# Kernel tuning notes

Measured on AMD Instinct MI355X. Metric: run time of the kernel, lower is better.

The kernel has to match this reference:

```python
import jax, jax.numpy as jnp
import numpy as np

H = 512
NHALF = 32  # N // 2 complex conjugate pairs
LLEN = 8192


def setup_inputs() -> dict:
    key = jax.random.key(0)
    k1, k2, k3 = jax.random.split(key, 3)
    # log_dt ~ uniform in [log(dt_min), log(dt_max)]
    log_dt = jax.random.uniform(k1, (H,), dtype=jnp.float32) * (
        np.log(0.1) - np.log(0.001)) + np.log(0.001)
    # C: complex randn stored as (H, NHALF, 2) real view
    C = jax.random.normal(k2, (H, NHALF, 2), dtype=jnp.float32)
    log_A_real = jnp.log(0.5 * jnp.ones((H, NHALF), dtype=jnp.float32))
    A_imag = np.pi * jnp.broadcast_to(
        jnp.arange(NHALF, dtype=jnp.float32), (H, NHALF))
    return {"C": C, "log_dt": log_dt, "log_A_real": log_A_real,
            "A_imag": A_imag, "L": LLEN}


def reference(C, log_dt, log_A_real, A_imag, L):
    # zoh discretization of diagonal SSM -> kernel K of shape (H, L)
    dt = jnp.exp(log_dt)                                  # (H,)
    Cc = (C[..., 0] + 1j * C[..., 1]).astype(jnp.complex64)  # (H, n)
    A = (-jnp.exp(log_A_real) + 1j * A_imag).astype(jnp.complex64)  # (H, n)
    dtA = A * dt[:, None]                                 # (H, n)
    t = jnp.arange(L, dtype=jnp.float32)                  # (L,)
    C_scaled = Cc * (jnp.exp(dtA) - 1.0) / A              # (H, n)
    # Vandermonde: exp(dtA)^t over length L, reduce over n
    T = jnp.exp(dtA[:, :, None] * t[None, None, :])       # (H, n, L) complex
    K = 2.0 * jnp.einsum('hn,hnl->hl', C_scaled, T).real  # (H, L)
    return K
```

## Files before the change

### kernel.cpp

```cpp
#include <hip/hip_runtime.h>
#include <math.h>

#define HDIM   512
#define NH     32
#define NP     16
#define LLEN   8192
#define BLOCK  256
#define LSPLIT 2
#define LPB    (LLEN / LSPLIT)
#define LPT    16

typedef float vf2 __attribute__((ext_vector_type(2)));

static __device__ inline vf2 pk_mul(vf2 a, vf2 b) {
    vf2 d; asm("v_pk_mul_f32 %0, %1, %2" : "=v"(d) : "v"(a), "v"(b)); return d;
}
static __device__ inline vf2 pk_add(vf2 a, vf2 b) {
    vf2 d; asm("v_pk_add_f32 %0, %1, %2" : "=v"(d) : "v"(a), "v"(b)); return d;
}
static __device__ inline vf2 pk_fma(vf2 a, vf2 b, vf2 c) {
    vf2 d; asm("v_pk_fma_f32 %0, %1, %2, %3" : "=v"(d) : "v"(a), "v"(b), "v"(c)); return d;
}
static __device__ inline vf2 pk_fms(vf2 a, vf2 b, vf2 c) {
    vf2 d; asm("v_pk_fma_f32 %0, %1, %2, %3 neg_lo:[0,0,1] neg_hi:[0,0,1]"
               : "=v"(d) : "v"(a), "v"(b), "v"(c)); return d;
}

__global__ __launch_bounds__(BLOCK) void s4d_kernel(
    const float* __restrict__ C,
    const float* __restrict__ log_dt,
    const float* __restrict__ log_A_real,
    const float* __restrict__ A_imag,
    float* __restrict__ out)
{
    __shared__ float4 tabA[NP + 1][16];
    __shared__ float4 tabB[NP + 1][16];
    __shared__ float4 s_w [NP + 1];
    __shared__ float4 s_pq[NP + 1];
    __shared__ float4 s_p2[NP + 1];

    const int h   = blockIdx.y;
    const int ls  = blockIdx.x;
    const int tid = threadIdx.x;

    {
        const int n = tid & 31;
        const int g = tid >> 5;
        const int P = n >> 1, o = n & 1;
        const double dt  = exp((double)log_dt[h]);
        const double Are = -exp((double)log_A_real[h * NH + n]);
        const double Aim = (double)A_imag[h * NH + n];
        const double dre = Are * dt, dim = Aim * dt;

        double s1, c1; sincos(dim, &s1, &c1);
        const double em  = exp(dre);
        const double w1r = em * c1, w1i = em * s1;

        float* tabAf = (float*)&tabA[0][0];
        float* tabBf = (float*)&tabB[0][0];

        if (g < 4) {
            const double nre = w1r - 1.0, nim = w1i;
            const double den = Are * Are + Aim * Aim;
            const double fre = (nre * Are + nim * Aim) / den;
            const double fim = (nim * Are - nre * Aim) / den;
            const double Cre = (double)C[(h * NH + n) * 2 + 0];
            const double Cim = (double)C[(h * NH + n) * 2 + 1];
            const double csr = 2.0 * (Cre * fre - Cim * fim);
            const double csi = 2.0 * (Cre * fim + Cim * fre);

            const int    i0   = g * 4;
            const double base = 16.0 * (double)i0;
            double s0, c0; sincos(dim * base, &s0, &c0);
            const double m0 = exp(dre * base);
            const double er = m0 * c0, ei = m0 * s0;
            double gr = csr * er - csi * ei;
            double gi = csr * ei + csi * er;
            double ss, cs; sincos(dim * 16.0, &ss, &cs);
            const double ms  = exp(dre * 16.0);
            const double str = ms * cs, sti = ms * ss;
            for (int k = 0; k < 4; ++k) {
                const int idx = (P * 16 + i0 + k) * 4;
                tabAf[idx + o]     = (float)gr;
                tabAf[idx + 2 + o] = (float)gi;
                const double t = gr * str - gi * sti;
                gi = gr * sti + gi * str;
                gr = t;
            }
        } else {
            const int    i0   = (g - 4) * 4;
            const double base = (double)(LPB * ls) + 256.0 * (double)i0;
            double s0, c0; sincos(dim * base, &s0, &c0);
            const double m0 = exp(dre * base);
            double er = m0 * c0, ei = m0 * s0;
            double ss, cs; sincos(dim * 256.0, &ss, &cs);
            const double ms  = exp(dre * 256.0);
            const double str = ms * cs, sti = ms * ss;
            for (int k = 0; k < 4; ++k) {
                const int idx = (P * 16 + i0 + k) * 4;
                tabBf[idx + o]     = (float)er;
                tabBf[idx + 2 + o] = (float)ei;
                const double t = er * str - ei * sti;
                ei = er * sti + ei * str;
                er = t;
            }
        }

        if (g == 0) {
            float* wf  = (float*)&s_w[0];
            float* pqf = (float*)&s_pq[0];
            float* p2f = (float*)&s_p2[0];
            const double p  = 2.0 * w1r;
            const double q  = em * em;
            const double p2 = 2.0 * (w1r * w1r - w1i * w1i);
            const double q2 = q * q;
            wf [P * 4 + o]     = (float)w1r;
            wf [P * 4 + 2 + o] = (float)w1i;
            pqf[P * 4 + o]     = (float)p;
            pqf[P * 4 + 2 + o] = (float)q;
            p2f[P * 4 + o]     = (float)p2;
            p2f[P * 4 + 2 + o] = (float)q2;
        }
    }
    __syncthreads();

    const int lo = tid & 15, hi = tid >> 4;

    vf2 acc[LPT];
#pragma unroll
    for (int l = 0; l < LPT; ++l) acc[l] = (vf2)(0.f);

    float4 a4 = tabA[0][lo], b4 = tabB[0][hi];
    float4 c0 = s_w[0], c1 = s_pq[0], c2 = s_p2[0];

#pragma unroll 2
    for (int P = 0; P < NP; ++P) {
        const float4 na = tabA[P + 1][lo], nb = tabB[P + 1][hi];
        const float4 n0 = s_w[P + 1], n1 = s_pq[P + 1], n2 = s_p2[P + 1];

        const vf2 Ax = {a4.x, a4.y}, Ay = {a4.z, a4.w};
        const vf2 Bx = {b4.x, b4.y}, By = {b4.z, b4.w};
        const vf2 wr = {c0.x, c0.y}, wi = {c0.z, c0.w};
        const vf2 p  = {c1.x, c1.y}, q  = {c1.z, c1.w};
        const vf2 p2 = {c2.x, c2.y}, q2 = {c2.z, c2.w};

        const vf2 Tr = pk_fms(Ax, Bx, pk_mul(Ay, By));
        const vf2 Ti = pk_fma(Ax, By, pk_mul(Ay, Bx));
        const vf2 y0 = Tr;
        const vf2 y1 = pk_fms(Tr, wr, pk_mul(Ti, wi));
        const vf2 y2 = pk_fms(p, y1, pk_mul(q, y0));
        const vf2 y3 = pk_fms(p, y2, pk_mul(q, y1));
        acc[0] = pk_add(acc[0], y0);
        acc[1] = pk_add(acc[1], y1);
        acc[2] = pk_add(acc[2], y2);
        acc[3] = pk_add(acc[3], y3);

        vf2 e0 = y0, e1 = y2, o0 = y1, o1 = y3;
#pragma unroll
        for (int m = 0; m < 6; ++m) {
            const vf2 e2 = pk_fms(p2, e1, pk_mul(q2, e0));
            const vf2 o2 = pk_fms(p2, o1, pk_mul(q2, o0));
            acc[4 + 2 * m] = pk_add(acc[4 + 2 * m], e2);
            acc[5 + 2 * m] = pk_add(acc[5 + 2 * m], o2);
            e0 = e1; e1 = e2;
            o0 = o1; o1 = o2;
        }
        a4 = na; b4 = nb; c0 = n0; c1 = n1; c2 = n2;
    }

    float* orow = out + (size_t)h * LLEN + ls * LPB + LPT * tid;
#pragma unroll
    for (int j = 0; j < 4; ++j) {
        *(float4*)(orow + 4 * j) = make_float4(
            acc[4*j+0].x + acc[4*j+0].y,
            acc[4*j+1].x + acc[4*j+1].y,
            acc[4*j+2].x + acc[4*j+2].y,
            acc[4*j+3].x + acc[4*j+3].y);
    }
}

extern "C" void kernel_launch(void* const* d_in, const int* in_sizes, int n_in,
                              void* d_out, int out_size, void* d_ws, size_t ws_size,
                              hipStream_t stream) {
    const float* C          = (const float*)d_in[0];
    const float* log_dt     = (const float*)d_in[1];
    const float* log_A_real = (const float*)d_in[2];
    const float* A_imag     = (const float*)d_in[3];
    float* out = (float*)d_out;

    dim3 grid(LSPLIT, HDIM);
    s4d_kernel<<<grid, BLOCK, 0, stream>>>(C, log_dt, log_A_real, A_imag, out);
}
```

Baseline: 76.77 us.

## Split double-precision table setup into separate precompute kernel feeding main kernel

Moves the per-head double-precision twiddle/table generation (sincos/exp) out of the main kernel into a separate kernel that writes the tables to workspace. It computes them once per head instead of once per L-split block, and uses repeated squaring instead of transcendental calls. The main kernel now only loads the tables from global memory into shared memory, and its launch bounds request higher occupancy. The cost is an extra kernel launch and a global-memory round trip. Long sequential complex-multiply chains in double precision replace the parallel sincos, which may also change accuracy slightly.

```diff
diff --git a/kernel.cpp b/kernel.cpp
--- a/kernel.cpp
+++ b/kernel.cpp
@@ -10,6 +10,12 @@
 #define LPB    (LLEN / LSPLIT)
 #define LPT    16
 
+#define OFF_A   0
+#define OFF_B   524288
+#define OFF_W   1572864
+#define OFF_PQ  1605632
+#define OFF_P2  1638400
+
 typedef float vf2 __attribute__((ext_vector_type(2)));
 
 static __device__ inline vf2 pk_mul(vf2 a, vf2 b) {
@@ -26,11 +32,91 @@
                : "=v"(d) : "v"(a), "v"(b), "v"(c)); return d;
 }
 
-__global__ __launch_bounds__(BLOCK) void s4d_kernel(
+__global__ __launch_bounds__(256) void s4d_tables(
     const float* __restrict__ C,
     const float* __restrict__ log_dt,
     const float* __restrict__ log_A_real,
     const float* __restrict__ A_imag,
+    float* __restrict__ ws)
+{
+    const int gid = blockIdx.x * 256 + threadIdx.x;
+    if (gid >= HDIM * NH * 3) return;
+    const int h    = gid / 96;
+    const int r    = gid - h * 96;
+    const int n    = r & 31;
+    const int walk = r >> 5;
+    const int P = n >> 1, o = n & 1;
+
+    const double dt  = exp((double)log_dt[h]);
+    const double Are = -exp((double)log_A_real[h * NH + n]);
+    const double Aim = (double)A_imag[h * NH + n];
+    const double dre = Are * dt, dim = Aim * dt;
+
+    double s1, c1; sincos(dim, &s1, &c1);
+    const double em = exp(dre);
+    const double wr = em * c1, wi = em * s1;
+
+    double xr = wr, xi = wi;
+#pragma unroll
+    for (int j = 0; j < 4; ++j) { const double t = xr*xr - xi*xi; xi = 2.0*xr*xi; xr = t; }
+
+    float* gA  = ws + OFF_A;
+    float* gB  = ws + OFF_B;
+    float* gW  = ws + OFF_W;
+    float* gPQ = ws + OFF_PQ;
+    float* gP2 = ws + OFF_P2;
+
+    if (walk == 0) {
+        const double p  = 2.0 * wr;
+        const double q  = em * em;
+        const double p2 = 2.0 * (wr * wr - wi * wi);
+        const double q2 = q * q;
+        gW [(h*16 + P)*4 + o]     = (float)wr;
+        gW [(h*16 + P)*4 + 2 + o] = (float)wi;
+        gPQ[(h*16 + P)*4 + o]     = (float)p;
+        gPQ[(h*16 + P)*4 + 2 + o] = (float)q;
+        gP2[(h*16 + P)*4 + o]     = (float)p2;
+        gP2[(h*16 + P)*4 + 2 + o] = (float)q2;
+
+        const double nre = wr - 1.0, nim = wi;
+        const double inv = 1.0 / (Are * Are + Aim * Aim);
+        const double fre = (nre * Are + nim * Aim) * inv;
+        const double fim = (nim * Are - nre * Aim) * inv;
+        const double Cre = (double)C[(h * NH + n) * 2 + 0];
+        const double Cim = (double)C[(h * NH + n) * 2 + 1];
+        double gr = 2.0 * (Cre * fre - Cim * fim);
+        double gi = 2.0 * (Cre * fim + Cim * fre);
+        for (int k = 0; k < 16; ++k) {
+            const int idx = (h * 256 + P * 16 + k) * 4;
+            gA[idx + o]     = (float)gr;
+            gA[idx + 2 + o] = (float)gi;
+            const double t = gr * xr - gi * xi;
+            gi = gr * xi + gi * xr; gr = t;
+        }
+    } else {
+#pragma unroll
+        for (int j = 0; j < 4; ++j) { const double t = xr*xr - xi*xi; xi = 2.0*xr*xi; xr = t; }
+        const int ls = walk - 1;
+        double er, ei;
+        if (ls == 0) { er = 1.0; ei = 0.0; }
+        else {
+            double br = xr, bi = xi;
+#pragma unroll
+            for (int j = 0; j < 4; ++j) { const double t = br*br - bi*bi; bi = 2.0*br*bi; br = t; }
+            er = br; ei = bi;
+        }
+        for (int k = 0; k < 16; ++k) {
+            const int idx = ((ls * 512 + h) * 256 + P * 16 + k) * 4;
+            gB[idx + o]     = (float)er;
+            gB[idx + 2 + o] = (float)ei;
+            const double t = er * xr - ei * xi;
+            ei = er * xi + ei * xr; er = t;
+        }
+    }
+}
+
+__global__ __launch_bounds__(BLOCK, 4) void s4d_main(
+    const float* __restrict__ ws,
     float* __restrict__ out)
 {
     __shared__ float4 tabA[NP + 1][16];
@@ -44,83 +130,16 @@
     const int tid = threadIdx.x;
 
     {
-        const int n = tid & 31;
-        const int g = tid >> 5;
-        const int P = n >> 1, o = n & 1;
-        const double dt  = exp((double)log_dt[h]);
-        const double Are = -exp((double)log_A_real[h * NH + n]);
-        const double Aim = (double)A_imag[h * NH + n];
-        const double dre = Are * dt, dim = Aim * dt;
-
-        double s1, c1; sincos(dim, &s1, &c1);
-        const double em  = exp(dre);
-        const double w1r = em * c1, w1i = em * s1;
-
-        float* tabAf = (float*)&tabA[0][0];
-        float* tabBf = (float*)&tabB[0][0];
-
-        if (g < 4) {
-            const double nre = w1r - 1.0, nim = w1i;
-            const double den = Are * Are + Aim * Aim;
-            const double fre = (nre * Are + nim * Aim) / den;
-            const double fim = (nim * Are - nre * Aim) / den;
-            const double Cre = (double)C[(h * NH + n) * 2 + 0];
-            const double Cim = (double)C[(h * NH + n) * 2 + 1];
-            const double csr = 2.0 * (Cre * fre - Cim * fim);
-            const double csi = 2.0 * (Cre * fim + Cim * fre);
-
-            const int    i0   = g * 4;
-            const double base = 16.0 * (double)i0;
-            double s0, c0; sincos(dim * base, &s0, &c0);
-            const double m0 = exp(dre * base);
-            const double er = m0 * c0, ei = m0 * s0;
-            double gr = csr * er - csi * ei;
-            double gi = csr * ei + csi * er;
-            double ss, cs; sincos(dim * 16.0, &ss, &cs);
-            const double ms  = exp(dre * 16.0);
-            const double str = ms * cs, sti = ms * ss;
-            for (int k = 0; k < 4; ++k) {
-                const int idx = (P * 16 + i0 + k) * 4;
-                tabAf[idx + o]     = (float)gr;
-                tabAf[idx + 2 + o] = (float)gi;
-                const double t = gr * str - gi * sti;
-                gi = gr * sti + gi * str;
-                gr = t;
-            }
-        } else {
-            const int    i0   = (g - 4) * 4;
-            const double base = (double)(LPB * ls) + 256.0 * (double)i0;
-            double s0, c0; sincos(dim * base, &s0, &c0);
-            const double m0 = exp(dre * base);
-            double er = m0 * c0, ei = m0 * s0;
-            double ss, cs; sincos(dim * 256.0, &ss, &cs);
-            const double ms  = exp(dre * 256.0);
-            const double str = ms * cs, sti = ms * ss;
-            for (int k = 0; k < 4; ++k) {
-                const int idx = (P * 16 + i0 + k) * 4;
-                tabBf[idx + o]     = (float)er;
-                tabBf[idx + 2 + o] = (float)ei;
-                const double t = er * str - ei * sti;
-                ei = er * sti + ei * str;
-                er = t;
-            }
-        }
-
-        if (g == 0) {
-            float* wf  = (float*)&s_w[0];
-            float* pqf = (float*)&s_pq[0];
-            float* p2f = (float*)&s_p2[0];
-            const double p  = 2.0 * w1r;
-            const double q  = em * em;
-            const double p2 = 2.0 * (w1r * w1r - w1i * w1i);
-            const double q2 = q * q;
-            wf [P * 4 + o]     = (float)w1r;
-            wf [P * 4 + 2 + o] = (float)w1i;
-            pqf[P * 4 + o]     = (float)p;
-            pqf[P * 4 + 2 + o] = (float)q;
-            p2f[P * 4 + o]     = (float)p2;
-            p2f[P * 4 + 2 + o] = (float)q2;
-        }
+        const float4* gA4  = (const float4*)(ws + OFF_A);
+        const float4* gB4  = (const float4*)(ws + OFF_B);
+        const float4* gW4  = (const float4*)(ws + OFF_W);
+        const float4* gPQ4 = (const float4*)(ws + OFF_PQ);
+        const float4* gP24 = (const float4*)(ws + OFF_P2);
+        ((float4*)&tabA[0][0])[tid] = gA4[h * 256 + tid];
+        ((float4*)&tabB[0][0])[tid] = gB4[(ls * 512 + h) * 256 + tid];
+        if (tid < 16)      s_w [tid]      = gW4 [h * 16 + tid];
+        else if (tid < 32) s_pq[tid - 16] = gPQ4[h * 16 + tid - 16];
+        else if (tid < 48) s_p2[tid - 32] = gP24[h * 16 + tid - 32];
     }
     __syncthreads();
 
@@ -187,7 +206,8 @@
     const float* log_A_real = (const float*)d_in[2];
     const float* A_imag     = (const float*)d_in[3];
     float* out = (float*)d_out;
-
-    dim3 grid(LSPLIT, HDIM);
-    s4d_kernel<<<grid, BLOCK, 0, stream>>>(C, log_dt, log_A_real, A_imag, out);
-}
+    float* ws  = (float*)d_ws;
+
+    s4d_tables<<<192, 256, 0, stream>>>(C, log_dt, log_A_real, A_imag, ws);
+    s4d_main<<<dim3(LSPLIT, HDIM), BLOCK, 0, stream>>>(ws, out);
+}
```

New measurement: 88.74 us. 15.6% more time.
